# Kernel tuning notes

Hardware: AMD Instinct MI355X
Metric: run time of the kernel (lower is better)

Reference implementation:

```python
import jax, jax.numpy as jnp
import numpy as np

B, T, H = 4096, 2048, 64  # batch, max seq len, hidden size
IN = 1                    # decoder input hardcoded to width 1 in source
BOT = 3                   # latent bottleneck (linear_enc: H->3, linear_dec: 3->H)


def setup_inputs() -> dict:
    key = jax.random.key(0)
    ks = jax.random.split(key, 16)
    s = 1.0 / np.sqrt(H)
    u = lambda k, shape: jax.random.uniform(k, shape, jnp.float32, -s, s)
    padded = jax.random.normal(ks[0], (B, T, IN), jnp.float32)
    seq_lengths = jax.random.randint(ks[1], (B,), 1, T + 1).at[0].set(T)  # max == T (static unroll)
    return {
        "padded": padded,
        "seq_lengths": seq_lengths,
        # encoder LSTM (gate order i,f,g,o like torch); biases b_ih+b_hh fused
        "enc_Wih": u(ks[2], (4 * H, IN)),
        "enc_Whh": u(ks[3], (4 * H, H)),
        "enc_b":   u(ks[4], (4 * H,)),
        # encoder bottleneck linear H->3
        "enc_linW": u(ks[5], (BOT, H)),
        "enc_linb": u(ks[6], (BOT,)),
        # decoder expand linear 3->H
        "dec_linW": u(ks[7], (H, BOT)),
        "dec_linb": u(ks[8], (H,)),
        # decoder LSTM
        "dec_Wih": u(ks[9], (4 * H, IN)),
        "dec_Whh": u(ks[10], (4 * H, H)),
        "dec_b":   u(ks[11], (4 * H,)),
        # output linear H->1
        "outW": u(ks[12], (IN, H)),
        "outb": u(ks[13], (IN,)),
    }


def _lstm_cell(x, h, c, Wih, Whh, b):
    g = x @ Wih.T + h @ Whh.T + b
    i, f, gg, o = jnp.split(g, 4, axis=-1)
    c = jax.nn.sigmoid(f) * c + jax.nn.sigmoid(i) * jnp.tanh(gg)
    h = jax.nn.sigmoid(o) * jnp.tanh(c)
    return h, c


def reference(padded, seq_lengths, enc_Wih, enc_Whh, enc_b, enc_linW, enc_linb,
              dec_linW, dec_linb, dec_Wih, dec_Whh, dec_b, outW, outb):
    Bn, Tn, _ = padded.shape
    Hn = enc_Whh.shape[1]
    xs = jnp.transpose(padded, (1, 0, 2))                       # (T, B, 1)
    mask = jnp.arange(Tn)[:, None] < seq_lengths[None, :]        # (T, B)

    # ---- encoder: packed semantics == freeze (h,c) past each seq's length ----
    h0 = jnp.zeros((Bn, Hn), padded.dtype)
    def enc_step(carry, xm):
        h, c = carry
        x, m = xm
        nh, nc = _lstm_cell(x, h, c, enc_Wih, enc_Whh, enc_b)
        m = m[:, None]
        return (jnp.where(m, nh, h), jnp.where(m, nc, c)), None
    (h, c), _ = jax.lax.scan(enc_step, (h0, h0), (xs, mask))

    hz = jax.nn.sigmoid(h @ enc_linW.T + enc_linb)               # (B, 3) latent

    hd = hz @ dec_linW.T + dec_linb                              # (B, H)
    x0 = jnp.zeros((Bn, 1), padded.dtype)
    def dec_step(carry, _):
        x, hh, cc = carry
        nh, nc = _lstm_cell(x, hh, cc, dec_Wih, dec_Whh, dec_b)
        y = nh @ outW.T + outb
        return (y, nh, nc), y
    _, ys = jax.lax.scan(dec_step, (x0, hd, c), None, length=Tn)  # (T, B, 1)
    output = jnp.transpose(ys, (1, 0, 2))                         # (B, T, 1)

    # ---- masked MSE ----
    maskf = mask.T[:, :, None].astype(padded.dtype)               # (B, T, 1)
    loss = (((padded - output) ** 2) * maskf).sum() / maskf.sum()
    return loss, padded, output, hz[None]
```

## Files before the change

kernel.cpp:

```cpp
#include <hip/hip_runtime.h>

#define B 4096
#define T 2048
#define H 64
#define NBATCH 8
#define NB (B / NBATCH)
#define NTHREADS 512

typedef __attribute__((ext_vector_type(8))) short short8;
typedef __attribute__((ext_vector_type(4))) float f32x4;

__device__ __forceinline__ float ex2(float x) { return __builtin_amdgcn_exp2f(x); }
__device__ __forceinline__ float sigm(float x) {
    return __builtin_amdgcn_rcpf(1.0f + ex2(-1.4426950408889634f * x));
}
__device__ __forceinline__ float tanh_(float x) {
    return __builtin_fmaf(2.0f,
        __builtin_amdgcn_rcpf(1.0f + ex2(-2.8853900817779268f * x)), -1.0f);
}
__device__ __forceinline__ unsigned short f2bf(float f) {
    unsigned u = __builtin_bit_cast(unsigned, f);
    u += 0x7fffu + ((u >> 16) & 1u);
    return (unsigned short)(u >> 16);
}
__device__ __forceinline__ void lds_barrier() {
    asm volatile("s_waitcnt lgkmcnt(0)\n\ts_barrier" ::: "memory");
}

extern "C" __global__ void __launch_bounds__(NTHREADS, 4)
enc_kernel(const float* __restrict__ padded, const int* __restrict__ seq_len,
           const float* __restrict__ Wih, const float* __restrict__ Whh,
           const float* __restrict__ bias,
           float* __restrict__ h_out, float* __restrict__ c_out)
{
    __shared__ unsigned short hA[2][NBATCH][72];
    __shared__ int slen[NBATCH];

    const int tid = threadIdx.x;
    const int w = tid >> 6, L = tid & 63, lo = L & 15, hi = L >> 4;
    const int b0 = blockIdx.x * NBATCH;
    const int bat = lo & 7;
    const bool hiT = lo >= 8;
    const int unit = w * 8 + (hiT ? 4 : 0) + hi;

    short8 af[2][2];
    #pragma unroll
    for (int rt = 0; rt < 2; ++rt) {
        const int G = (lo & 3) * 64 + w * 8 + rt * 4 + (lo >> 2);
        #pragma unroll
        for (int kk = 0; kk < 2; ++kk) {
            const float* src = Whh + (long)G * H + kk * 32 + hi * 8;
            short8 f;
            #pragma unroll
            for (int j = 0; j < 8; ++j) f[j] = (short)f2bf(src[j]);
            af[rt][kk] = f;
        }
    }
    float b_g[2][4], wi_g[2][4];
    #pragma unroll
    for (int rt = 0; rt < 2; ++rt)
        #pragma unroll
        for (int r = 0; r < 4; ++r) {
            const int G2 = r * 64 + w * 8 + rt * 4 + hi;
            b_g[rt][r] = bias[G2];
            wi_g[rt][r] = Wih[G2];
        }

    hA[0][tid >> 6][tid & 63] = 0;
    if (tid < NBATCH) slen[tid] = seq_len[b0 + tid];
    lds_barrier();

    int maxlen = 1;
    #pragma unroll
    for (int i = 0; i < NBATCH; ++i) maxlen = max(maxlen, slen[i]);
    const int len_lo = slen[bat];

    const float* xrow = padded + (long)(b0 + bat) * T;
    f32x4 xc = *(const f32x4*)(xrow);
    f32x4 xn = *(const f32x4*)(xrow + 4);

    float c_st = 0.f, h_st = 0.f;

#define ESTEP(P, XI)                                                          \
    {                                                                         \
        const float x = xc[XI];                                               \
        short8 hb0 = *(const short8*)&hA[P][bat][hi * 8];                     \
        short8 hb1 = *(const short8*)&hA[P][bat][32 + hi * 8];                \
        f32x4 z0 = {b_g[0][0] + wi_g[0][0] * x, b_g[0][1] + wi_g[0][1] * x,   \
                    b_g[0][2] + wi_g[0][2] * x, b_g[0][3] + wi_g[0][3] * x};  \
        f32x4 z1 = {b_g[1][0] + wi_g[1][0] * x, b_g[1][1] + wi_g[1][1] * x,   \
                    b_g[1][2] + wi_g[1][2] * x, b_g[1][3] + wi_g[1][3] * x};  \
        z0 = __builtin_amdgcn_mfma_f32_16x16x32_bf16(af[0][0], hb0, z0, 0,0,0); \
        z1 = __builtin_amdgcn_mfma_f32_16x16x32_bf16(af[1][0], hb0, z1, 0,0,0); \
        z0 = __builtin_amdgcn_mfma_f32_16x16x32_bf16(af[0][1], hb1, z0, 0,0,0); \
        z1 = __builtin_amdgcn_mfma_f32_16x16x32_bf16(af[1][1], hb1, z1, 0,0,0); \
        const bool act = (t + XI) < len_lo;                                   \
        const float a0 = hiT ? z1[0] : z0[0];                                 \
        const float a1 = hiT ? z1[1] : z0[1];                                 \
        const float a2 = hiT ? z1[2] : z0[2];                                 \
        const float a3 = hiT ? z1[3] : z0[3];                                 \
        float i_ = sigm(a0);                                                  \
        float f_ = sigm(a1);                                                  \
        float g_ = tanh_(a2);                                                 \
        float o_ = sigm(a3);                                                  \
        float cn = f_ * c_st + i_ * g_;                                       \
        float hn = o_ * tanh_(cn);                                            \
        if (act) { c_st = cn; h_st = hn; }                                    \
        hA[(P) ^ 1][bat][unit] = f2bf(h_st);                                  \
        lds_barrier();                                                        \
    }

    for (int t = 0; t < maxlen; t += 4) {
        int nb = t + 8; if (nb > T - 4) nb = T - 4;
        f32x4 xf = *(const f32x4*)(xrow + nb);
        ESTEP(0, 0) ESTEP(1, 1) ESTEP(0, 2) ESTEP(1, 3)
        xc = xn; xn = xf;
    }
#undef ESTEP

    h_out[(long)(b0 + bat) * H + unit] = h_st;
    c_out[(long)(b0 + bat) * H + unit] = c_st;
}

extern "C" __global__ void __launch_bounds__(256)
mid_kernel(const float* __restrict__ h_enc,
           const float* __restrict__ eW, const float* __restrict__ eb,
           const float* __restrict__ dW, const float* __restrict__ db,
           const float* __restrict__ outW, const float* __restrict__ outb,
           float* __restrict__ hz_out, float* __restrict__ hd_out,
           float* __restrict__ y0c)
{
    int b = blockIdx.x * blockDim.x + threadIdx.x;
    if (b >= B) return;
    const float* h = h_enc + (long)b * H;
    float hz[3];
    #pragma unroll
    for (int j = 0; j < 3; ++j) {
        float s = eb[j];
        for (int k = 0; k < H; ++k) s += h[k] * eW[j*H + k];
        hz[j] = sigm(s);
        hz_out[b*3 + j] = hz[j];
    }
    float y0 = outb[0];
    for (int u = 0; u < H; ++u) {
        float hd = db[u] + hz[0]*dW[u*3] + hz[1]*dW[u*3+1] + hz[2]*dW[u*3+2];
        hd_out[(long)b*H + u] = hd;
        y0 += outW[u] * hd;
    }
    y0c[b] = y0;
}

extern "C" __global__ void __launch_bounds__(NTHREADS, 4)
dec_kernel(const float* __restrict__ hd, const float* __restrict__ c_in,
           const float* __restrict__ Wih, const float* __restrict__ Whh,
           const float* __restrict__ bias, const float* __restrict__ outW,
           const float* __restrict__ outb, const float* __restrict__ y0c,
           float* __restrict__ y_out)
{
    __shared__ unsigned short hA[2][NBATCH][72];

    const int tid = threadIdx.x;
    const int w = tid >> 6, L = tid & 63, lo = L & 15, hi = L >> 4;
    const int b0 = blockIdx.x * NBATCH;
    const int bat = lo & 7;
    const bool hiT = lo >= 8;
    const int unit = w * 8 + (hiT ? 4 : 0) + hi;

    short8 af[2][2];
    #pragma unroll
    for (int rt = 0; rt < 2; ++rt) {
        const int G = (lo & 3) * 64 + w * 8 + rt * 4 + (lo >> 2);
        const float wir = Wih[G];
        #pragma unroll
        for (int kk = 0; kk < 2; ++kk) {
            const float* src = Whh + (long)G * H + kk * 32 + hi * 8;
            const float* ow  = outW + kk * 32 + hi * 8;
            short8 f;
            #pragma unroll
            for (int j = 0; j < 8; ++j) f[j] = (short)f2bf(src[j] + wir * ow[j]);
            af[rt][kk] = f;
        }
    }
    const float outb_s = outb[0];
    const float y0 = y0c[b0 + bat];
    float zb[2][4];
    #pragma unroll
    for (int rt = 0; rt < 2; ++rt)
        #pragma unroll
        for (int r = 0; r < 4; ++r) {
            const int G2 = r * 64 + w * 8 + rt * 4 + hi;
            zb[rt][r] = bias[G2] + Wih[G2] * outb_s;
        }
    float corr[4];
    #pragma unroll
    for (int r = 0; r < 4; ++r)
        corr[r] = Wih[r * 64 + unit] * y0;

    short8 ya[2];
    #pragma unroll
    for (int kk = 0; kk < 2; ++kk) {
        short8 f = (short8)0;
        if (lo == 0)
            #pragma unroll
            for (int j = 0; j < 8; ++j) f[j] = (short)f2bf(outW[kk*32 + hi*8 + j]);
        ya[kk] = f;
    }

    hA[0][tid >> 6][tid & 63] = f2bf(hd[(long)(b0 + (tid >> 6)) * H + (tid & 63)]);
    float c_st = c_in[(long)(b0 + bat) * H + unit];
    lds_barrier();

#define DSTEP(P, CORR, TT)                                                    \
    {                                                                         \
        short8 hb0 = *(const short8*)&hA[P][bat][hi * 8];                     \
        short8 hb1 = *(const short8*)&hA[P][bat][32 + hi * 8];                \
        f32x4 z0 = {zb[0][0], zb[0][1], zb[0][2], zb[0][3]};                  \
        f32x4 z1 = {zb[1][0], zb[1][1], zb[1][2], zb[1][3]};                  \
        z0 = __builtin_amdgcn_mfma_f32_16x16x32_bf16(af[0][0], hb0, z0, 0,0,0); \
        z1 = __builtin_amdgcn_mfma_f32_16x16x32_bf16(af[1][0], hb0, z1, 0,0,0); \
        z0 = __builtin_amdgcn_mfma_f32_16x16x32_bf16(af[0][1], hb1, z0, 0,0,0); \
        z1 = __builtin_amdgcn_mfma_f32_16x16x32_bf16(af[1][1], hb1, z1, 0,0,0); \
        if (w == ((TT) & 7)) {      \
            f32x4 zy = {outb_s, outb_s, outb_s, outb_s};                      \
            zy = __builtin_amdgcn_mfma_f32_16x16x32_bf16(ya[0], hb0, zy, 0,0,0); \
            zy = __builtin_amdgcn_mfma_f32_16x16x32_bf16(ya[1], hb1, zy, 0,0,0); \
            if ((TT) > 0 && hi == 0 && lo < 8)                                \
                y_out[(long)(b0 + lo) * T + ((TT) - 1)] = zy[0];              \
        }                                                                     \
        float a0 = hiT ? z1[0] : z0[0];                                       \
        float a1 = hiT ? z1[1] : z0[1];                                       \
        float a2 = hiT ? z1[2] : z0[2];                                       \
        float a3 = hiT ? z1[3] : z0[3];                                       \
        if (CORR) { a0 -= corr[0]; a1 -= corr[1]; a2 -= corr[2]; a3 -= corr[3]; } \
        float i_ = sigm(a0);                                                  \
        float f_ = sigm(a1);                                                  \
        float g_ = tanh_(a2);                                                 \
        float o_ = sigm(a3);                                                  \
        float cn = f_ * c_st + i_ * g_;                                       \
        float hn = o_ * tanh_(cn);                                            \
        c_st = cn;                                                            \
        hA[(P) ^ 1][bat][unit] = f2bf(hn);                                    \
        lds_barrier();                                                        \
    }

    DSTEP(0, 1, 0) DSTEP(1, 0, 1) DSTEP(0, 0, 2) DSTEP(1, 0, 3)
    for (int t = 4; t < T; t += 4) {
        DSTEP(0, 0, t) DSTEP(1, 0, t + 1) DSTEP(0, 0, t + 2) DSTEP(1, 0, t + 3)
    }
#undef DSTEP

    if (w == 0) {
        short8 hb0 = *(const short8*)&hA[0][bat][hi * 8];
        short8 hb1 = *(const short8*)&hA[0][bat][32 + hi * 8];
        f32x4 zy = {outb_s, outb_s, outb_s, outb_s};
        zy = __builtin_amdgcn_mfma_f32_16x16x32_bf16(ya[0], hb0, zy, 0,0,0);
        zy = __builtin_amdgcn_mfma_f32_16x16x32_bf16(ya[1], hb1, zy, 0,0,0);
        if (hi == 0 && lo < 8) y_out[(long)(b0 + lo) * T + (T - 1)] = zy[0];
    }
}

extern "C" __global__ void __launch_bounds__(256)
loss_kernel(const float* __restrict__ padded, const float* __restrict__ y,
            const int* __restrict__ seq_len, float* __restrict__ acc2)
{
    const long n4 = (long)B * T / 4;
    long i0 = (long)(blockIdx.x * blockDim.x + threadIdx.x);
    long stride = (long)gridDim.x * blockDim.x;
    float s = 0.f, cnt = 0.f;
    for (long i = i0; i < n4; i += stride) {
        int b = (int)(i >> 9);
        int t = (int)(i & 511) * 4;
        int len = seq_len[b];
        f32x4 pv = *(const f32x4*)&padded[i * 4];
        f32x4 yv = *(const f32x4*)&y[i * 4];
        #pragma unroll
        for (int e = 0; e < 4; ++e)
            if (t + e < len) { float d = pv[e] - yv[e]; s += d * d; cnt += 1.0f; }
    }
    for (int m = 1; m < 64; m <<= 1) { s += __shfl_xor(s, m); cnt += __shfl_xor(cnt, m); }
    if ((threadIdx.x & 63) == 0) { atomicAdd(&acc2[0], s); atomicAdd(&acc2[1], cnt); }
}

extern "C" __global__ void fin_kernel(const float* __restrict__ acc2, float* __restrict__ out)
{
    out[0] = acc2[0] / acc2[1];
}

extern "C" void kernel_launch(void* const* d_in, const int* in_sizes, int n_in,
                              void* d_out, int out_size, void* d_ws, size_t ws_size,
                              hipStream_t stream)
{
    const float* padded = (const float*)d_in[0];
    const int*   seq    = (const int*)  d_in[1];
    const float* eWih   = (const float*)d_in[2];
    const float* eWhh   = (const float*)d_in[3];
    const float* eb     = (const float*)d_in[4];
    const float* elW    = (const float*)d_in[5];
    const float* elb    = (const float*)d_in[6];
    const float* dlW    = (const float*)d_in[7];
    const float* dlb    = (const float*)d_in[8];
    const float* dWih   = (const float*)d_in[9];
    const float* dWhh   = (const float*)d_in[10];
    const float* db     = (const float*)d_in[11];
    const float* outW   = (const float*)d_in[12];
    const float* outb   = (const float*)d_in[13];
    float* out = (float*)d_out;

    float* ws    = (float*)d_ws;
    float* h_enc = ws;
    float* c_enc = ws + (long)B * H;
    float* hd    = ws + 2L * B * H;
    float* y0c   = ws + 3L * B * H;
    float* acc2  = ws + 3L * B * H + B;

    float* out_pad = out + 1;
    float* out_y   = out + 1 + (long)B * T;
    float* out_hz  = out + 1 + 2L * (long)B * T;

    hipMemcpyAsync(out_pad, padded, (long)B * T * sizeof(float),
                   hipMemcpyDeviceToDevice, stream);
    hipMemsetAsync(acc2, 0, 2 * sizeof(float), stream);

    enc_kernel<<<NB, NTHREADS, 0, stream>>>(padded, seq, eWih, eWhh, eb, h_enc, c_enc);
    mid_kernel<<<B / 256, 256, 0, stream>>>(h_enc, elW, elb, dlW, dlb, outW, outb,
                                            out_hz, hd, y0c);
    dec_kernel<<<NB, NTHREADS, 0, stream>>>(hd, c_enc, dWih, dWhh, db, outW, outb, y0c, out_y);
    loss_kernel<<<1024, 256, 0, stream>>>(padded, out_y, seq, acc2);
    fin_kernel<<<1, 1, 0, stream>>>(acc2, out);
}
```

Before: 2.077 ms.

## Fill all 16 MFMA columns with distinct batch rows, halving block count

Each block now processes 16 sequences instead of 8, so the N=16 dimension of the 16x16x32 MFMA carries real batch rows rather than duplicated ones. Each lane now computes gate activations for two hidden units, and the pair is packed into bf16 with a single v_cvt_pk_bf16_f32. This halves the number of blocks and the total MFMA and barrier work per sequence. In exchange, each lane does twice the transcendental work per step, and occupancy drops to 2 blocks per CU with fewer blocks overall. The encoder's maxlen now spans 16 sequences, which adds padding steps.

Result: faster. 1.828 ms (-12.0%).

```diff
diff --git a/kernel.cpp b/kernel.cpp
--- a/kernel.cpp
+++ b/kernel.cpp
@@ -3,7 +3,7 @@
 #define B 4096
 #define T 2048
 #define H 64
-#define NBATCH 8
+#define NBATCH 16
 #define NB (B / NBATCH)
 #define NTHREADS 512
 
@@ -23,25 +23,29 @@
     u += 0x7fffu + ((u >> 16) & 1u);
     return (unsigned short)(u >> 16);
 }
+__device__ __forceinline__ unsigned pk_bf16(float a, float b) {
+    unsigned r;
+    asm("v_cvt_pk_bf16_f32 %0, %1, %2" : "=v"(r) : "v"(a), "v"(b));
+    return r;
+}
 __device__ __forceinline__ void lds_barrier() {
     asm volatile("s_waitcnt lgkmcnt(0)\n\ts_barrier" ::: "memory");
 }
 
-extern "C" __global__ void __launch_bounds__(NTHREADS, 4)
+extern "C" __global__ void __launch_bounds__(NTHREADS, 2)
 enc_kernel(const float* __restrict__ padded, const int* __restrict__ seq_len,
            const float* __restrict__ Wih, const float* __restrict__ Whh,
            const float* __restrict__ bias,
            float* __restrict__ h_out, float* __restrict__ c_out)
 {
-    __shared__ unsigned short hA[2][NBATCH][72];
+    __shared__ unsigned short hX[2][NBATCH][72];
     __shared__ int slen[NBATCH];
 
     const int tid = threadIdx.x;
     const int w = tid >> 6, L = tid & 63, lo = L & 15, hi = L >> 4;
     const int b0 = blockIdx.x * NBATCH;
-    const int bat = lo & 7;
-    const bool hiT = lo >= 8;
-    const int unit = w * 8 + (hiT ? 4 : 0) + hi;
+    const int unitA = w * 8 + hi;
+    const int unitB = w * 8 + 4 + hi;
 
     short8 af[2][2];
     #pragma unroll
@@ -66,26 +70,28 @@
             wi_g[rt][r] = Wih[G2];
         }
 
-    hA[0][tid >> 6][tid & 63] = 0;
+    #pragma unroll
+    for (int idx = tid; idx < NBATCH * 64; idx += NTHREADS)
+        hX[0][idx >> 6][idx & 63] = 0;
     if (tid < NBATCH) slen[tid] = seq_len[b0 + tid];
     lds_barrier();
 
     int maxlen = 1;
     #pragma unroll
     for (int i = 0; i < NBATCH; ++i) maxlen = max(maxlen, slen[i]);
-    const int len_lo = slen[bat];
-
-    const float* xrow = padded + (long)(b0 + bat) * T;
+    const int len_lo = slen[lo];
+
+    const float* xrow = padded + (long)(b0 + lo) * T;
     f32x4 xc = *(const f32x4*)(xrow);
     f32x4 xn = *(const f32x4*)(xrow + 4);
 
-    float c_st = 0.f, h_st = 0.f;
+    float csA = 0.f, hsA = 0.f, csB = 0.f, hsB = 0.f;
 
 #define ESTEP(P, XI)                                                          \
     {                                                                         \
         const float x = xc[XI];                                               \
-        short8 hb0 = *(const short8*)&hA[P][bat][hi * 8];                     \
-        short8 hb1 = *(const short8*)&hA[P][bat][32 + hi * 8];                \
+        short8 hb0 = *(const short8*)&hX[P][lo][hi * 8];                      \
+        short8 hb1 = *(const short8*)&hX[P][lo][32 + hi * 8];                 \
         f32x4 z0 = {b_g[0][0] + wi_g[0][0] * x, b_g[0][1] + wi_g[0][1] * x,   \
                     b_g[0][2] + wi_g[0][2] * x, b_g[0][3] + wi_g[0][3] * x};  \
         f32x4 z1 = {b_g[1][0] + wi_g[1][0] * x, b_g[1][1] + wi_g[1][1] * x,   \
@@ -95,18 +101,18 @@
         z0 = __builtin_amdgcn_mfma_f32_16x16x32_bf16(af[0][1], hb1, z0, 0,0,0); \
         z1 = __builtin_amdgcn_mfma_f32_16x16x32_bf16(af[1][1], hb1, z1, 0,0,0); \
         const bool act = (t + XI) < len_lo;                                   \
-        const float a0 = hiT ? z1[0] : z0[0];                                 \
-        const float a1 = hiT ? z1[1] : z0[1];                                 \
-        const float a2 = hiT ? z1[2] : z0[2];                                 \
-        const float a3 = hiT ? z1[3] : z0[3];                                 \
-        float i_ = sigm(a0);                                                  \
-        float f_ = sigm(a1);                                                  \
-        float g_ = tanh_(a2);                                                 \
-        float o_ = sigm(a3);                                                  \
-        float cn = f_ * c_st + i_ * g_;                                       \
-        float hn = o_ * tanh_(cn);                                            \
-        if (act) { c_st = cn; h_st = hn; }                                    \
-        hA[(P) ^ 1][bat][unit] = f2bf(h_st);                                  \
+        float iA = sigm(z0[0]), fA = sigm(z0[1]);                             \
+        float gA = tanh_(z0[2]), oA = sigm(z0[3]);                            \
+        float iB = sigm(z1[0]), fB = sigm(z1[1]);                             \
+        float gB = tanh_(z1[2]), oB = sigm(z1[3]);                            \
+        float cnA = fA * csA + iA * gA;                                       \
+        float cnB = fB * csB + iB * gB;                                       \
+        float hnA = oA * tanh_(cnA);                                          \
+        float hnB = oB * tanh_(cnB);                                          \
+        if (act) { csA = cnA; hsA = hnA; csB = cnB; hsB = hnB; }              \
+        unsigned up = pk_bf16(hsA, hsB);                                      \
+        hX[(P) ^ 1][lo][unitA] = (unsigned short)up;                          \
+        hX[(P) ^ 1][lo][unitB] = (unsigned short)(up >> 16);                  \
         lds_barrier();                                                        \
     }
 
@@ -118,8 +124,10 @@
     }
 #undef ESTEP
 
-    h_out[(long)(b0 + bat) * H + unit] = h_st;
-    c_out[(long)(b0 + bat) * H + unit] = c_st;
+    h_out[(long)(b0 + lo) * H + unitA] = hsA;
+    h_out[(long)(b0 + lo) * H + unitB] = hsB;
+    c_out[(long)(b0 + lo) * H + unitA] = csA;
+    c_out[(long)(b0 + lo) * H + unitB] = csB;
 }
 
 extern "C" __global__ void __launch_bounds__(256)
@@ -150,21 +158,20 @@
     y0c[b] = y0;
 }
 
-extern "C" __global__ void __launch_bounds__(NTHREADS, 4)
+extern "C" __global__ void __launch_bounds__(NTHREADS, 2)
 dec_kernel(const float* __restrict__ hd, const float* __restrict__ c_in,
            const float* __restrict__ Wih, const float* __restrict__ Whh,
            const float* __restrict__ bias, const float* __restrict__ outW,
            const float* __restrict__ outb, const float* __restrict__ y0c,
            float* __restrict__ y_out)
 {
-    __shared__ unsigned short hA[2][NBATCH][72];
+    __shared__ unsigned short hX[2][NBATCH][72];
 
     const int tid = threadIdx.x;
     const int w = tid >> 6, L = tid & 63, lo = L & 15, hi = L >> 4;
     const int b0 = blockIdx.x * NBATCH;
-    const int bat = lo & 7;
-    const bool hiT = lo >= 8;
-    const int unit = w * 8 + (hiT ? 4 : 0) + hi;
+    const int unitA = w * 8 + hi;
+    const int unitB = w * 8 + 4 + hi;
 
     short8 af[2][2];
     #pragma unroll
@@ -182,19 +189,16 @@
         }
     }
     const float outb_s = outb[0];
-    const float y0 = y0c[b0 + bat];
-    float zb[2][4];
+    const float y0 = y0c[b0 + lo];
+    float zb[2][4], corr[2][4];
     #pragma unroll
     for (int rt = 0; rt < 2; ++rt)
         #pragma unroll
         for (int r = 0; r < 4; ++r) {
             const int G2 = r * 64 + w * 8 + rt * 4 + hi;
             zb[rt][r] = bias[G2] + Wih[G2] * outb_s;
+            corr[rt][r] = Wih[G2] * y0;
         }
-    float corr[4];
-    #pragma unroll
-    for (int r = 0; r < 4; ++r)
-        corr[r] = Wih[r * 64 + unit] * y0;
 
     short8 ya[2];
     #pragma unroll
@@ -206,14 +210,17 @@
         ya[kk] = f;
     }
 
-    hA[0][tid >> 6][tid & 63] = f2bf(hd[(long)(b0 + (tid >> 6)) * H + (tid & 63)]);
-    float c_st = c_in[(long)(b0 + bat) * H + unit];
+    #pragma unroll
+    for (int idx = tid; idx < NBATCH * 64; idx += NTHREADS)
+        hX[0][idx >> 6][idx & 63] = f2bf(hd[(long)(b0 + (idx >> 6)) * H + (idx & 63)]);
+    float csA = c_in[(long)(b0 + lo) * H + unitA];
+    float csB = c_in[(long)(b0 + lo) * H + unitB];
     lds_barrier();
 
 #define DSTEP(P, CORR, TT)                                                    \
     {                                                                         \
-        short8 hb0 = *(const short8*)&hA[P][bat][hi * 8];                     \
-        short8 hb1 = *(const short8*)&hA[P][bat][32 + hi * 8];                \
+        short8 hb0 = *(const short8*)&hX[P][lo][hi * 8];                      \
+        short8 hb1 = *(const short8*)&hX[P][lo][32 + hi * 8];                 \
         f32x4 z0 = {zb[0][0], zb[0][1], zb[0][2], zb[0][3]};                  \
         f32x4 z1 = {zb[1][0], zb[1][1], zb[1][2], zb[1][3]};                  \
         z0 = __builtin_amdgcn_mfma_f32_16x16x32_bf16(af[0][0], hb0, z0, 0,0,0); \
@@ -224,22 +231,25 @@
             f32x4 zy = {outb_s, outb_s, outb_s, outb_s};                      \
             zy = __builtin_amdgcn_mfma_f32_16x16x32_bf16(ya[0], hb0, zy, 0,0,0); \
             zy = __builtin_amdgcn_mfma_f32_16x16x32_bf16(ya[1], hb1, zy, 0,0,0); \
-            if ((TT) > 0 && hi == 0 && lo < 8)                                \
+            if ((TT) > 0 && hi == 0)                                          \
                 y_out[(long)(b0 + lo) * T + ((TT) - 1)] = zy[0];              \
         }                                                                     \
-        float a0 = hiT ? z1[0] : z0[0];                                       \
-        float a1 = hiT ? z1[1] : z0[1];                                       \
-        float a2 = hiT ? z1[2] : z0[2];                                       \
-        float a3 = hiT ? z1[3] : z0[3];                                       \
-        if (CORR) { a0 -= corr[0]; a1 -= corr[1]; a2 -= corr[2]; a3 -= corr[3]; } \
-        float i_ = sigm(a0);                                                  \
-        float f_ = sigm(a1);                                                  \
-        float g_ = tanh_(a2);                                                 \
-        float o_ = sigm(a3);                                                  \
-        float cn = f_ * c_st + i_ * g_;                                       \
-        float hn = o_ * tanh_(cn);                                            \
-        c_st = cn;                                                            \
-        hA[(P) ^ 1][bat][unit] = f2bf(hn);                                    \
+        if (CORR) {                                                           \
+            _Pragma("unroll")                                                 \
+            for (int r = 0; r < 4; ++r) { z0[r] -= corr[0][r]; z1[r] -= corr[1][r]; } \
+        }                                                                     \
+        float iA = sigm(z0[0]), fA = sigm(z0[1]);                             \
+        float gA = tanh_(z0[2]), oA = sigm(z0[3]);                            \
+        float iB = sigm(z1[0]), fB = sigm(z1[1]);                             \
+        float gB = tanh_(z1[2]), oB = sigm(z1[3]);                            \
+        float cnA = fA * csA + iA * gA;                                       \
+        float cnB = fB * csB + iB * gB;                                       \
+        float hnA = oA * tanh_(cnA);                                          \
+        float hnB = oB * tanh_(cnB);                                          \
+        csA = cnA; csB = cnB;                                                 \
+        unsigned up = pk_bf16(hnA, hnB);                                      \
+        hX[(P) ^ 1][lo][unitA] = (unsigned short)up;                          \
+        hX[(P) ^ 1][lo][unitB] = (unsigned short)(up >> 16);                  \
         lds_barrier();                                                        \
     }
 
@@ -250,12 +260,12 @@
 #undef DSTEP
 
     if (w == 0) {
-        short8 hb0 = *(const short8*)&hA[0][bat][hi * 8];
-        short8 hb1 = *(const short8*)&hA[0][bat][32 + hi * 8];
+        short8 hb0 = *(const short8*)&hX[0][lo][hi * 8];
+        short8 hb1 = *(const short8*)&hX[0][lo][32 + hi * 8];
         f32x4 zy = {outb_s, outb_s, outb_s, outb_s};
         zy = __builtin_amdgcn_mfma_f32_16x16x32_bf16(ya[0], hb0, zy, 0,0,0);
         zy = __builtin_amdgcn_mfma_f32_16x16x32_bf16(ya[1], hb1, zy, 0,0,0);
-        if (hi == 0 && lo < 8) y_out[(long)(b0 + lo) * T + (T - 1)] = zy[0];
+        if (hi == 0) y_out[(long)(b0 + lo) * T + (T - 1)] = zy[0];
     }
 }
 
```
